# Kernel tuning notes

Hardware: AMD Instinct MI355X
Metric: run time of the kernel (lower is better)

## Reference

```python
import jax, jax.numpy as jnp
import numpy as np

SEQ, N, D, E = 16, 50000, 128, 1600000  # seq_len, n_nodes (lstm batch), feature dim, n_edges


def setup_inputs() -> dict:
    key = jax.random.key(0)
    ks = jax.random.split(key, 12)
    s = 1.0 / np.sqrt(D)

    def unif(k, shape):
        return jax.random.uniform(k, shape, jnp.float32, -s, s)

    return {
        "input_aux": jax.random.normal(ks[0], (SEQ, N, D), jnp.float32),
        "edges": jax.random.randint(ks[1], (2, E), 0, N, dtype=jnp.int64),
        # PyTorch LSTM params (single layer): gates ordered [i, f, g, o]
        "W_ih": unif(ks[2], (4 * D, D)),
        "W_hh": unif(ks[3], (4 * D, D)),
        "b_ih": unif(ks[4], (4 * D,)),
        "b_hh": unif(ks[5], (4 * D,)),
        # GCNConv layers (normalize=False): x' = scatter_sum((x @ W)[src] -> dst) + b
        "W1": unif(ks[6], (D, D)),
        "b1": unif(ks[7], (D,)),
        "W2": unif(ks[8], (D, D)),
        "b2": unif(ks[9], (D,)),
    }


def _lstm_last_hidden(x, W_ih, W_hh, b_ih, b_hh):
    # x: [T, N, D] (batch_first=False). Returns final hidden state h_T: [N, H].
    H = W_hh.shape[1]
    b = b_ih + b_hh

    def step(carry, xt):
        h, c = carry
        gates = xt @ W_ih.T + h @ W_hh.T + b  # [N, 4H]
        i, f, g, o = jnp.split(gates, 4, axis=-1)
        i = jax.nn.sigmoid(i)
        f = jax.nn.sigmoid(f)
        g = jnp.tanh(g)
        o = jax.nn.sigmoid(o)
        c = f * c + i * g
        h = o * jnp.tanh(c)
        return (h, c), None

    h0 = jnp.zeros((x.shape[1], H), x.dtype)
    (h, _), _ = jax.lax.scan(step, (h0, h0), x)
    return h


def _gcn_conv(x, edges, W, b):
    # GCNConv with normalize=False: transform, gather from source, scatter-sum to target, add bias.
    xw = x @ W                                    # [N, D]
    msg = xw[edges[0]]                            # [E, D] gather
    out = jax.ops.segment_sum(msg, edges[1], num_segments=x.shape[0])  # [N, D] scatter
    return out + b


def reference(input_aux, W_ih, W_hh, b_ih, b_hh, W1, b1, W2, b2, edges):
    h = _lstm_last_hidden(input_aux, W_ih, W_hh, b_ih, b_hh)  # squeeze(hn): [N, D]
    x = jax.nn.relu(_gcn_conv(h, edges, W1, b1))
    return _gcn_conv(x, edges, W2, b2)
```

## Files before the change

### kernel.cpp

```cpp
#include <hip/hip_runtime.h>
#include <hip/hip_bf16.h>

#define D 128
#define G4 512
#define KK 256

typedef __attribute__((ext_vector_type(4))) float f32x4;
typedef __attribute__((ext_vector_type(8))) __bf16 bf16x8;
typedef __attribute__((ext_vector_type(8))) unsigned short u16x8;
typedef __attribute__((ext_vector_type(4))) unsigned int u32x4;

__device__ __forceinline__ float sigm2(float x) {
    return __builtin_amdgcn_rcpf(1.0f + __builtin_amdgcn_exp2f(-1.4426950408889634f * x));
}
__device__ __forceinline__ float tanh2(float x) {
    return 1.0f - 2.0f * __builtin_amdgcn_rcpf(1.0f + __builtin_amdgcn_exp2f(2.8853900817779268f * x));
}
__device__ __forceinline__ float bf_lo(unsigned int u) { return __uint_as_float(u << 16); }
__device__ __forceinline__ float bf_hi(unsigned int u) { return __uint_as_float(u & 0xffff0000u); }

__global__ void k_prep(const float* __restrict__ Wih, const float* __restrict__ Whh,
                       const float* __restrict__ bih, const float* __restrict__ bhh,
                       const float* __restrict__ W1, const float* __restrict__ W2,
                       __bf16* __restrict__ Wcomb, __bf16* __restrict__ W1t,
                       __bf16* __restrict__ W2t, float* __restrict__ bcomb) {
    int t = blockIdx.x * blockDim.x + threadIdx.x;
    if (t < G4 * KK) {
        int row = t / KK, k = t % KK;
        float v = (k < D) ? Wih[row * D + k] : Whh[row * D + (k - D)];
        Wcomb[t] = (__bf16)v;
    } else if (t < G4 * KK + D * D) {
        int u = t - G4 * KK; int o = u / D, k = u % D;
        W1t[u] = (__bf16)W1[k * D + o];
    } else if (t < G4 * KK + 2 * D * D) {
        int u = t - G4 * KK - D * D; int o = u / D, k = u % D;
        W2t[u] = (__bf16)W2[k * D + o];
    } else if (t < G4 * KK + 2 * D * D + G4) {
        int u = t - G4 * KK - 2 * D * D;
        bcomb[u] = bih[u] + bhh[u];
    }
}

__global__ __launch_bounds__(512, 1) void k_lstm3(
        const float* __restrict__ xin, const __bf16* __restrict__ Wcomb,
        const float* __restrict__ bcomb, const __bf16* __restrict__ W1t,
        __bf16* __restrict__ xw1, int n, int tsteps, int npairs, int nchunks) {
    __shared__ __bf16 xb[2][2][16][D];
    __shared__ __bf16 hb[2][2][16][D];

    const int tid = threadIdx.x;
    const int wid = tid >> 6, l = tid & 63, q = l >> 4, c16 = l & 15;
    const int dim = wid * 16 + c16;

    bf16x8 Wf[4][8];
#pragma unroll
    for (int g = 0; g < 4; ++g)
#pragma unroll
        for (int kb = 0; kb < 8; ++kb)
            Wf[g][kb] = *(const bf16x8*)(Wcomb + (size_t)(g * D + dim) * KK + kb * 32 + q * 8);
#pragma unroll
    for (int g = 0; g < 4; ++g)
#pragma unroll
        for (int kb = 0; kb < 8; ++kb) {
            f32x4 tmp = __builtin_bit_cast(f32x4, Wf[g][kb]);
            asm volatile("" : "+v"(tmp));
            Wf[g][kb] = __builtin_bit_cast(bf16x8, tmp);
        }

    const float bI = bcomb[0 * D + dim], bF = bcomb[1 * D + dim],
                bG = bcomb[2 * D + dim], bO = bcomb[3 * D + dim];

    const int sid = tid >> 8;
    const int su = tid & 255;
    const int srow = su >> 4, sc8 = (su & 15) * 8;
    const int fin = tsteps & 1;

    for (int p = blockIdx.x; p < npairs; p += gridDim.x) {
        const int cA = 2 * p, cB = 2 * p + 1;
        const bool hasB = (cB < nchunks);
        const int myc = sid ? (hasB ? cB : cA) : cA;

        ((float4*)&hb[sid][0][0][0])[su] = make_float4(0.f, 0.f, 0.f, 0.f);
        {
            const float* xp = xin + ((size_t)(myc * 16 + srow)) * D + sc8;
            float4 v0 = *(const float4*)xp, v1 = *(const float4*)(xp + 4);
            bf16x8 b;
            b[0] = (__bf16)v0.x; b[1] = (__bf16)v0.y; b[2] = (__bf16)v0.z; b[3] = (__bf16)v0.w;
            b[4] = (__bf16)v1.x; b[5] = (__bf16)v1.y; b[6] = (__bf16)v1.z; b[7] = (__bf16)v1.w;
            *(bf16x8*)&xb[sid][0][srow][sc8 ^ ((srow & 7) << 3)] = b;
        }
        __syncthreads();

        float csA[4] = {0.f, 0.f, 0.f, 0.f}, csB[4] = {0.f, 0.f, 0.f, 0.f};

        for (int t = 0; t < tsteps; ++t) {
            const int cur = t & 1, nxt = cur ^ 1;

            bf16x8 aA[8], aB[8];
#pragma unroll
            for (int kb = 0; kb < 4; ++kb) {
                const int e = (kb * 32 + q * 8) ^ ((c16 & 7) << 3);
                aA[kb]     = *(const bf16x8*)&xb[0][cur][c16][e];
                aA[4 + kb] = *(const bf16x8*)&hb[0][cur][c16][e];
                aB[kb]     = *(const bf16x8*)&xb[1][cur][c16][e];
                aB[4 + kb] = *(const bf16x8*)&hb[1][cur][c16][e];
            }

            float4 p0, p1;
            const bool pf = (t + 1 < tsteps);
            if (pf) {
                const float* xp = xin + ((size_t)(t + 1) * n + myc * 16 + srow) * D + sc8;
                p0 = *(const float4*)xp; p1 = *(const float4*)(xp + 4);
            }

            f32x4 accA[4] = {{0,0,0,0},{0,0,0,0},{0,0,0,0},{0,0,0,0}};
            f32x4 accB[4] = {{0,0,0,0},{0,0,0,0},{0,0,0,0},{0,0,0,0}};
#pragma unroll
            for (int kb = 0; kb < 8; ++kb)
#pragma unroll
                for (int g = 0; g < 4; ++g) {
                    accA[g] = __builtin_amdgcn_mfma_f32_16x16x32_bf16(aA[kb], Wf[g][kb], accA[g], 0, 0, 0);
                    accB[g] = __builtin_amdgcn_mfma_f32_16x16x32_bf16(aB[kb], Wf[g][kb], accB[g], 0, 0, 0);
                }

            if (pf) {
                bf16x8 b;
                b[0] = (__bf16)p0.x; b[1] = (__bf16)p0.y; b[2] = (__bf16)p0.z; b[3] = (__bf16)p0.w;
                b[4] = (__bf16)p1.x; b[5] = (__bf16)p1.y; b[6] = (__bf16)p1.z; b[7] = (__bf16)p1.w;
                *(bf16x8*)&xb[sid][nxt][srow][sc8 ^ ((srow & 7) << 3)] = b;
            }

#pragma unroll
            for (int j = 0; j < 4; ++j) {
                const int node = j + q * 4;
                {
                    float iv = sigm2(accA[0][j] + bI);
                    float fv = sigm2(accA[1][j] + bF);
                    float gv = tanh2(accA[2][j] + bG);
                    float ov = sigm2(accA[3][j] + bO);
                    float c = fv * csA[j] + iv * gv;
                    csA[j] = c;
                    hb[0][nxt][node][dim ^ ((node & 7) << 3)] = (__bf16)(ov * tanh2(c));
                }
                {
                    float iv = sigm2(accB[0][j] + bI);
                    float fv = sigm2(accB[1][j] + bF);
                    float gv = tanh2(accB[2][j] + bG);
                    float ov = sigm2(accB[3][j] + bO);
                    float c = fv * csB[j] + iv * gv;
                    csB[j] = c;
                    hb[1][nxt][node][dim ^ ((node & 7) << 3)] = (__bf16)(ov * tanh2(c));
                }
            }
            __syncthreads();
        }

        bf16x8 hA[4], hB[4];
#pragma unroll
        for (int kb = 0; kb < 4; ++kb) {
            const int e = (kb * 32 + q * 8) ^ ((c16 & 7) << 3);
            hA[kb] = *(const bf16x8*)&hb[0][fin][c16][e];
            hB[kb] = *(const bf16x8*)&hb[1][fin][c16][e];
        }
        f32x4 eA = {0,0,0,0}, eB = {0,0,0,0};
#pragma unroll
        for (int kb = 0; kb < 4; ++kb) {
            bf16x8 wf = *(const bf16x8*)(W1t + (size_t)dim * D + kb * 32 + q * 8);
            eA = __builtin_amdgcn_mfma_f32_16x16x32_bf16(hA[kb], wf, eA, 0, 0, 0);
            eB = __builtin_amdgcn_mfma_f32_16x16x32_bf16(hB[kb], wf, eB, 0, 0, 0);
        }
#pragma unroll
        for (int j = 0; j < 4; ++j) {
            const int node = j + q * 4;
            xb[0][1][node][dim] = (__bf16)eA[j];
            xb[1][1][node][dim] = (__bf16)eB[j];
        }
        __syncthreads();
        if (!(sid == 1 && !hasB))
            *(bf16x8*)(xw1 + (size_t)(myc * 16 + srow) * D + sc8) = *(const bf16x8*)&xb[sid][1][srow][sc8];
        __syncthreads();
    }
}

__global__ __launch_bounds__(256) void k_gemm2(
        const __bf16* __restrict__ in, const __bf16* __restrict__ Wt,
        __bf16* __restrict__ outm, int n) {
    const int tid = threadIdx.x, wid = tid >> 6, l = tid & 63, q = l >> 4, c16 = l & 15;
    const int R = (blockIdx.x * 4 + wid) * 16;
    if (R + 16 > n) return;
    bf16x8 af[4];
#pragma unroll
    for (int kb = 0; kb < 4; ++kb)
        af[kb] = *(const bf16x8*)(in + (size_t)(R + c16) * D + kb * 32 + q * 8);
#pragma unroll
    for (int nt = 0; nt < 8; ++nt) {
        f32x4 acc = {0, 0, 0, 0};
#pragma unroll
        for (int kb = 0; kb < 4; ++kb) {
            const __bf16* wb = Wt + (size_t)(nt * 16 + c16) * D + (kb * 32 + q * 8);
            acc = __builtin_amdgcn_mfma_f32_16x16x32_bf16(af[kb], *(const bf16x8*)wb, acc, 0, 0, 0);
        }
#pragma unroll
        for (int j = 0; j < 4; ++j)
            outm[(size_t)(R + q * 4 + j) * D + nt * 16 + c16] = (__bf16)acc[j];
    }
}

__global__ void k_hist(const int* __restrict__ dst, int* __restrict__ counts, int e) {
    for (int i = blockIdx.x * blockDim.x + threadIdx.x; i < e; i += gridDim.x * blockDim.x)
        atomicAdd(&counts[dst[i]], 1);
}
__global__ __launch_bounds__(1024) void k_scan1(const int* __restrict__ counts,
        int* __restrict__ offsets, int* __restrict__ bsum, int n) {
    __shared__ int sd[1024];
    int tid = threadIdx.x, i = blockIdx.x * 1024 + tid;
    int v = (i < n) ? counts[i] : 0;
    sd[tid] = v; __syncthreads();
    for (int off = 1; off < 1024; off <<= 1) {
        int t = (tid >= off) ? sd[tid - off] : 0; __syncthreads();
        sd[tid] += t; __syncthreads();
    }
    if (i < n) offsets[i] = sd[tid] - v;
    if (tid == 1023) bsum[blockIdx.x] = sd[1023];
}
__global__ void k_scan2(const int* __restrict__ bsum, int* __restrict__ bpref, int nb) {
    if (threadIdx.x == 0) {
        int run = 0;
        for (int i = 0; i < nb; ++i) { bpref[i] = run; run += bsum[i]; }
    }
}
__global__ __launch_bounds__(1024) void k_scan3(int* __restrict__ offsets,
        int* __restrict__ cursor, const int* __restrict__ bpref, int n, int e) {
    int i = blockIdx.x * 1024 + threadIdx.x;
    if (i < n) {
        int v = offsets[i] + bpref[blockIdx.x];
        offsets[i] = v; cursor[i] = v;
    }
    if (i == 0) offsets[n] = e;
}
__global__ void k_permute(const int* __restrict__ src, const int* __restrict__ dst,
                          int* cursor, int* __restrict__ csr, int e) {
    for (int i = blockIdx.x * blockDim.x + threadIdx.x; i < e; i += gridDim.x * blockDim.x) {
        int p = atomicAdd(&cursor[dst[i]], 1);
        csr[p] = src[i];
    }
}

template <bool OUT_F32, bool RELU>
__global__ __launch_bounds__(256) void k_gather3(const __bf16* __restrict__ xw,
        const int* __restrict__ offsets, const int* __restrict__ csr,
        const float* __restrict__ bias, void* __restrict__ outp, int n) {
    const int gg = (blockIdx.x << 4) | (threadIdx.x >> 4);
    const int l = threadIdx.x & 15;
    if (gg >= n) return;
    const int s = offsets[gg], e = offsets[gg + 1];
    const u32x4* __restrict__ xq = (const u32x4*)xw;
    float a[8] = {0,0,0,0,0,0,0,0};
    int i = s;
    for (; i + 4 <= e; i += 4) {
        u32x4 v0 = xq[(size_t)csr[i]     * 16 + l];
        u32x4 v1 = xq[(size_t)csr[i + 1] * 16 + l];
        u32x4 v2 = xq[(size_t)csr[i + 2] * 16 + l];
        u32x4 v3 = xq[(size_t)csr[i + 3] * 16 + l];
#pragma unroll
        for (int k = 0; k < 4; ++k) {
            a[2 * k]     += (bf_lo(v0[k]) + bf_lo(v1[k])) + (bf_lo(v2[k]) + bf_lo(v3[k]));
            a[2 * k + 1] += (bf_hi(v0[k]) + bf_hi(v1[k])) + (bf_hi(v2[k]) + bf_hi(v3[k]));
        }
    }
    for (; i < e; ++i) {
        u32x4 v = xq[(size_t)csr[i] * 16 + l];
#pragma unroll
        for (int k = 0; k < 4; ++k) { a[2 * k] += bf_lo(v[k]); a[2 * k + 1] += bf_hi(v[k]); }
    }
    const float4 b0 = *(const float4*)(bias + l * 8);
    const float4 b1 = *(const float4*)(bias + l * 8 + 4);
    float r[8] = {a[0] + b0.x, a[1] + b0.y, a[2] + b0.z, a[3] + b0.w,
                  a[4] + b1.x, a[5] + b1.y, a[6] + b1.z, a[7] + b1.w};
    if (RELU) {
#pragma unroll
        for (int k = 0; k < 8; ++k) r[k] = fmaxf(r[k], 0.f);
    }
    if (OUT_F32) {
        float* o = (float*)outp + (size_t)gg * D + l * 8;
        *(float4*)o       = make_float4(r[0], r[1], r[2], r[3]);
        *(float4*)(o + 4) = make_float4(r[4], r[5], r[6], r[7]);
    } else {
        bf16x8 b;
#pragma unroll
        for (int k = 0; k < 8; ++k) b[k] = (__bf16)r[k];
        *(bf16x8*)((__bf16*)outp + (size_t)gg * D + l * 8) = b;
    }
}

extern "C" void kernel_launch(void* const* d_in, const int* in_sizes, int n_in,
                              void* d_out, int out_size, void* d_ws, size_t ws_size,
                              hipStream_t stream) {
    const float* xin = (const float*)d_in[0];
    const int*   edges = (const int*)d_in[1];
    const float* Wih = (const float*)d_in[2];
    const float* Whh = (const float*)d_in[3];
    const float* bih = (const float*)d_in[4];
    const float* bhh = (const float*)d_in[5];
    const float* W1  = (const float*)d_in[6];
    const float* b1  = (const float*)d_in[7];
    const float* W2  = (const float*)d_in[8];
    const float* b2  = (const float*)d_in[9];
    float* outp = (float*)d_out;

    const int E = in_sizes[1] / 2;
    const int n = out_size / D;
    const int tsteps = in_sizes[0] / (n * D);
    const int* srcE = edges;
    const int* dstE = edges + E;

    char* ws = (char*)d_ws;
    size_t off = 0;
    auto alloc = [&](size_t bytes) { void* p = ws + off; off += (bytes + 511) & ~(size_t)511; return p; };
    __bf16* Wcomb = (__bf16*)alloc((size_t)G4 * KK * 2);
    __bf16* W1t   = (__bf16*)alloc((size_t)D * D * 2);
    __bf16* W2t   = (__bf16*)alloc((size_t)D * D * 2);
    float*  bcomb = (float*)alloc((size_t)G4 * 4);
    int* counts  = (int*)alloc((size_t)(n + 1) * 4);
    int* offsets = (int*)alloc((size_t)(n + 1) * 4);
    int* cursor  = (int*)alloc((size_t)(n + 1) * 4);
    int* bsum    = (int*)alloc(64 * 4);
    int* bpref   = (int*)alloc(64 * 4);
    int* csr     = (int*)alloc((size_t)E * 4);
    __bf16* xw1  = (__bf16*)alloc((size_t)n * D * 2);
    __bf16* out1 = (__bf16*)alloc((size_t)n * D * 2);
    __bf16* xw2  = xw1;
    (void)ws_size; (void)n_in;

    {
        int total = G4 * KK + 2 * D * D + G4;
        k_prep<<<(total + 255) / 256, 256, 0, stream>>>(Wih, Whh, bih, bhh, W1, W2,
                                                        Wcomb, W1t, W2t, bcomb);
    }
    hipMemsetAsync(counts, 0, (size_t)n * 4, stream);
    k_hist<<<2048, 256, 0, stream>>>(dstE, counts, E);
    int nb = (n + 1023) / 1024;
    k_scan1<<<nb, 1024, 0, stream>>>(counts, offsets, bsum, n);
    k_scan2<<<1, 64, 0, stream>>>(bsum, bpref, nb);
    k_scan3<<<nb, 1024, 0, stream>>>(offsets, cursor, bpref, n, E);
    k_permute<<<2048, 256, 0, stream>>>(srcE, dstE, cursor, csr, E);

    const int nchunks = n / 16;
    const int npairs = (nchunks + 1) / 2;
    k_lstm3<<<256, 512, 0, stream>>>(xin, Wcomb, bcomb, W1t, xw1, n, tsteps, npairs, nchunks);

    k_gather3<false, true><<<(n + 15) / 16, 256, 0, stream>>>(xw1, offsets, csr, b1, out1, n);
    k_gemm2<<<((n / 16) + 3) / 4, 256, 0, stream>>>(out1, W2t, xw2, n);
    k_gather3<true, false><<<(n + 15) / 16, 256, 0, stream>>>(xw2, offsets, csr, b2, outp, n);
}
```

Measured before the change: 1.043 ms.

## Restructure LSTM kernel with AGPR weights, transposed MFMA, padded LDS, wider gather unroll

The LSTM kernel now pins the recurrent weights in accumulator registers through inline-asm MFMA, and swaps operand order so each lane writes four consecutive hidden dims as one vector store. It also replaces the XOR swizzle with padded LDS rows, seeds the accumulators with biases held in shared memory, unrolls the time loop by two, and raises launch bounds to allow two blocks per CU. The GCN gather now issues eight neighbor loads per iteration to raise memory-level parallelism. Risks include register pressure from the doubled occupancy target, the hand-placed s_nop hazard padding, and the time loop assuming an even tsteps.

```diff
diff --git a/kernel.cpp b/kernel.cpp
--- a/kernel.cpp
+++ b/kernel.cpp
@@ -4,11 +4,17 @@
 #define D 128
 #define G4 512
 #define KK 256
+#define LROW 144
 
 typedef __attribute__((ext_vector_type(4))) float f32x4;
 typedef __attribute__((ext_vector_type(8))) __bf16 bf16x8;
-typedef __attribute__((ext_vector_type(8))) unsigned short u16x8;
+typedef __attribute__((ext_vector_type(4))) __bf16 bf16x4;
 typedef __attribute__((ext_vector_type(4))) unsigned int u32x4;
+
+#define MFMA_AV(acc, wf, xf) \
+    asm volatile("v_mfma_f32_16x16x32_bf16 %0, %1, %2, %0" : "+v"(acc) : "a"(wf), "v"(xf))
+#define MFMA_VV(acc, wf, xf) \
+    asm volatile("v_mfma_f32_16x16x32_bf16 %0, %1, %2, %0" : "+v"(acc) : "v"(wf), "v"(xf))
 
 __device__ __forceinline__ float sigm2(float x) {
     return __builtin_amdgcn_rcpf(1.0f + __builtin_amdgcn_exp2f(-1.4426950408889634f * x));
@@ -41,143 +47,144 @@
     }
 }
 
-__global__ __launch_bounds__(512, 1) void k_lstm3(
+__global__ __launch_bounds__(512, 2) void k_lstm4(
         const float* __restrict__ xin, const __bf16* __restrict__ Wcomb,
         const float* __restrict__ bcomb, const __bf16* __restrict__ W1t,
         __bf16* __restrict__ xw1, int n, int tsteps, int npairs, int nchunks) {
-    __shared__ __bf16 xb[2][2][16][D];
-    __shared__ __bf16 hb[2][2][16][D];
+    __shared__ __align__(16) float  sbias[G4];
+    __shared__ __align__(16) __bf16 xb[2][2][16][LROW];
+    __shared__ __align__(16) __bf16 hb[2][2][16][LROW];
 
     const int tid = threadIdx.x;
     const int wid = tid >> 6, l = tid & 63, q = l >> 4, c16 = l & 15;
-    const int dim = wid * 16 + c16;
+    const int q8 = q * 8;
+    const int wrow = wid * 16 + c16;
+    const int w16q4 = wid * 16 + q * 4;
 
     bf16x8 Wf[4][8];
 #pragma unroll
     for (int g = 0; g < 4; ++g)
 #pragma unroll
         for (int kb = 0; kb < 8; ++kb)
-            Wf[g][kb] = *(const bf16x8*)(Wcomb + (size_t)(g * D + dim) * KK + kb * 32 + q * 8);
-#pragma unroll
-    for (int g = 0; g < 4; ++g)
-#pragma unroll
-        for (int kb = 0; kb < 8; ++kb) {
-            f32x4 tmp = __builtin_bit_cast(f32x4, Wf[g][kb]);
-            asm volatile("" : "+v"(tmp));
-            Wf[g][kb] = __builtin_bit_cast(bf16x8, tmp);
-        }
-
-    const float bI = bcomb[0 * D + dim], bF = bcomb[1 * D + dim],
-                bG = bcomb[2 * D + dim], bO = bcomb[3 * D + dim];
+            Wf[g][kb] = *(const bf16x8*)(Wcomb + (size_t)(g * D + wrow) * KK + kb * 32 + q8);
+
+    if (tid < G4) sbias[tid] = bcomb[tid];
 
     const int sid = tid >> 8;
     const int su = tid & 255;
     const int srow = su >> 4, sc8 = (su & 15) * 8;
-    const int fin = tsteps & 1;
 
     for (int p = blockIdx.x; p < npairs; p += gridDim.x) {
         const int cA = 2 * p, cB = 2 * p + 1;
         const bool hasB = (cB < nchunks);
         const int myc = sid ? (hasB ? cB : cA) : cA;
 
-        ((float4*)&hb[sid][0][0][0])[su] = make_float4(0.f, 0.f, 0.f, 0.f);
         {
+            bf16x8 z = {};
+            *(bf16x8*)&hb[sid][0][srow][sc8] = z;
             const float* xp = xin + ((size_t)(myc * 16 + srow)) * D + sc8;
             float4 v0 = *(const float4*)xp, v1 = *(const float4*)(xp + 4);
             bf16x8 b;
             b[0] = (__bf16)v0.x; b[1] = (__bf16)v0.y; b[2] = (__bf16)v0.z; b[3] = (__bf16)v0.w;
             b[4] = (__bf16)v1.x; b[5] = (__bf16)v1.y; b[6] = (__bf16)v1.z; b[7] = (__bf16)v1.w;
-            *(bf16x8*)&xb[sid][0][srow][sc8 ^ ((srow & 7) << 3)] = b;
+            *(bf16x8*)&xb[sid][0][srow][sc8] = b;
         }
         __syncthreads();
 
         float csA[4] = {0.f, 0.f, 0.f, 0.f}, csB[4] = {0.f, 0.f, 0.f, 0.f};
 
-        for (int t = 0; t < tsteps; ++t) {
-            const int cur = t & 1, nxt = cur ^ 1;
-
-            bf16x8 aA[8], aB[8];
-#pragma unroll
-            for (int kb = 0; kb < 4; ++kb) {
-                const int e = (kb * 32 + q * 8) ^ ((c16 & 7) << 3);
-                aA[kb]     = *(const bf16x8*)&xb[0][cur][c16][e];
-                aA[4 + kb] = *(const bf16x8*)&hb[0][cur][c16][e];
-                aB[kb]     = *(const bf16x8*)&xb[1][cur][c16][e];
-                aB[4 + kb] = *(const bf16x8*)&hb[1][cur][c16][e];
+        for (int t0 = 0; t0 < tsteps; t0 += 2) {
+#pragma unroll
+            for (int tt = 0; tt < 2; ++tt) {
+                const int t = t0 + tt, cur = tt, nxt = tt ^ 1;
+
+                f32x4 accA[4], accB[4];
+#pragma unroll
+                for (int g = 0; g < 4; ++g) {
+                    accA[g] = *(const f32x4*)&sbias[g * D + w16q4];
+                    accB[g] = accA[g];
+                }
+
+                float4 px0, px1;
+                const bool pf = (t + 1 < tsteps);
+                if (pf) {
+                    const float* xp = xin + ((size_t)(t + 1) * n + myc * 16 + srow) * D + sc8;
+                    px0 = *(const float4*)xp; px1 = *(const float4*)(xp + 4);
+                }
+
+#pragma unroll
+                for (int kb = 0; kb < 8; ++kb) {
+                    const int e = (kb & 3) * 32 + q8;
+                    bf16x8 fA, fB;
+                    if (kb < 4) {
+                        fA = *(const bf16x8*)&xb[0][cur][c16][e];
+                        fB = *(const bf16x8*)&xb[1][cur][c16][e];
+                    } else {
+                        fA = *(const bf16x8*)&hb[0][cur][c16][e];
+                        fB = *(const bf16x8*)&hb[1][cur][c16][e];
+                    }
+                    MFMA_AV(accA[0], Wf[0][kb], fA); MFMA_AV(accB[0], Wf[0][kb], fB);
+                    MFMA_AV(accA[1], Wf[1][kb], fA); MFMA_AV(accB[1], Wf[1][kb], fB);
+                    MFMA_AV(accA[2], Wf[2][kb], fA); MFMA_AV(accB[2], Wf[2][kb], fB);
+                    MFMA_AV(accA[3], Wf[3][kb], fA); MFMA_AV(accB[3], Wf[3][kb], fB);
+                }
+                asm volatile("s_nop 7\n\ts_nop 7");
+
+                if (pf) {
+                    bf16x8 b;
+                    b[0] = (__bf16)px0.x; b[1] = (__bf16)px0.y; b[2] = (__bf16)px0.z; b[3] = (__bf16)px0.w;
+                    b[4] = (__bf16)px1.x; b[5] = (__bf16)px1.y; b[6] = (__bf16)px1.z; b[7] = (__bf16)px1.w;
+                    *(bf16x8*)&xb[sid][nxt][srow][sc8] = b;
+                }
+
+                {
+                    bf16x4 hv;
+#pragma unroll
+                    for (int j = 0; j < 4; ++j) {
+                        float iv = sigm2(accA[0][j]);
+                        float fv = sigm2(accA[1][j]);
+                        float gv = tanh2(accA[2][j]);
+                        float ov = sigm2(accA[3][j]);
+                        float c = fv * csA[j] + iv * gv;
+                        csA[j] = c;
+                        hv[j] = (__bf16)(ov * tanh2(c));
+                    }
+                    *(bf16x4*)&hb[0][nxt][c16][w16q4] = hv;
+                }
+                {
+                    bf16x4 hv;
+#pragma unroll
+                    for (int j = 0; j < 4; ++j) {
+                        float iv = sigm2(accB[0][j]);
+                        float fv = sigm2(accB[1][j]);
+                        float gv = tanh2(accB[2][j]);
+                        float ov = sigm2(accB[3][j]);
+                        float c = fv * csB[j] + iv * gv;
+                        csB[j] = c;
+                        hv[j] = (__bf16)(ov * tanh2(c));
+                    }
+                    *(bf16x4*)&hb[1][nxt][c16][w16q4] = hv;
+                }
+                __syncthreads();
             }
-
-            float4 p0, p1;
-            const bool pf = (t + 1 < tsteps);
-            if (pf) {
-                const float* xp = xin + ((size_t)(t + 1) * n + myc * 16 + srow) * D + sc8;
-                p0 = *(const float4*)xp; p1 = *(const float4*)(xp + 4);
-            }
-
-            f32x4 accA[4] = {{0,0,0,0},{0,0,0,0},{0,0,0,0},{0,0,0,0}};
-            f32x4 accB[4] = {{0,0,0,0},{0,0,0,0},{0,0,0,0},{0,0,0,0}};
-#pragma unroll
-            for (int kb = 0; kb < 8; ++kb)
-#pragma unroll
-                for (int g = 0; g < 4; ++g) {
-                    accA[g] = __builtin_amdgcn_mfma_f32_16x16x32_bf16(aA[kb], Wf[g][kb], accA[g], 0, 0, 0);
-                    accB[g] = __builtin_amdgcn_mfma_f32_16x16x32_bf16(aB[kb], Wf[g][kb], accB[g], 0, 0, 0);
-                }
-
-            if (pf) {
-                bf16x8 b;
-                b[0] = (__bf16)p0.x; b[1] = (__bf16)p0.y; b[2] = (__bf16)p0.z; b[3] = (__bf16)p0.w;
-                b[4] = (__bf16)p1.x; b[5] = (__bf16)p1.y; b[6] = (__bf16)p1.z; b[7] = (__bf16)p1.w;
-                *(bf16x8*)&xb[sid][nxt][srow][sc8 ^ ((srow & 7) << 3)] = b;
-            }
-
-#pragma unroll
-            for (int j = 0; j < 4; ++j) {
-                const int node = j + q * 4;
-                {
-                    float iv = sigm2(accA[0][j] + bI);
-                    float fv = sigm2(accA[1][j] + bF);
-                    float gv = tanh2(accA[2][j] + bG);
-                    float ov = sigm2(accA[3][j] + bO);
-                    float c = fv * csA[j] + iv * gv;
-                    csA[j] = c;
-                    hb[0][nxt][node][dim ^ ((node & 7) << 3)] = (__bf16)(ov * tanh2(c));
-                }
-                {
-                    float iv = sigm2(accB[0][j] + bI);
-                    float fv = sigm2(accB[1][j] + bF);
-                    float gv = tanh2(accB[2][j] + bG);
-                    float ov = sigm2(accB[3][j] + bO);
-                    float c = fv * csB[j] + iv * gv;
-                    csB[j] = c;
-                    hb[1][nxt][node][dim ^ ((node & 7) << 3)] = (__bf16)(ov * tanh2(c));
-                }
-            }
-            __syncthreads();
-        }
-
-        bf16x8 hA[4], hB[4];
+        }
+
+        f32x4 eA = {0, 0, 0, 0}, eB = {0, 0, 0, 0};
 #pragma unroll
         for (int kb = 0; kb < 4; ++kb) {
-            const int e = (kb * 32 + q * 8) ^ ((c16 & 7) << 3);
-            hA[kb] = *(const bf16x8*)&hb[0][fin][c16][e];
-            hB[kb] = *(const bf16x8*)&hb[1][fin][c16][e];
-        }
-        f32x4 eA = {0,0,0,0}, eB = {0,0,0,0};
-#pragma unroll
-        for (int kb = 0; kb < 4; ++kb) {
-            bf16x8 wf = *(const bf16x8*)(W1t + (size_t)dim * D + kb * 32 + q * 8);
-            eA = __builtin_amdgcn_mfma_f32_16x16x32_bf16(hA[kb], wf, eA, 0, 0, 0);
-            eB = __builtin_amdgcn_mfma_f32_16x16x32_bf16(hB[kb], wf, eB, 0, 0, 0);
-        }
-#pragma unroll
-        for (int j = 0; j < 4; ++j) {
-            const int node = j + q * 4;
-            xb[0][1][node][dim] = (__bf16)eA[j];
-            xb[1][1][node][dim] = (__bf16)eB[j];
-        }
-        __syncthreads();
-        if (!(sid == 1 && !hasB))
-            *(bf16x8*)(xw1 + (size_t)(myc * 16 + srow) * D + sc8) = *(const bf16x8*)&xb[sid][1][srow][sc8];
+            bf16x8 w1f = *(const bf16x8*)(W1t + (size_t)wrow * D + kb * 32 + q8);
+            bf16x8 hA = *(const bf16x8*)&hb[0][0][c16][kb * 32 + q8];
+            bf16x8 hB = *(const bf16x8*)&hb[1][0][c16][kb * 32 + q8];
+            MFMA_VV(eA, w1f, hA);
+            MFMA_VV(eB, w1f, hB);
+        }
+        asm volatile("s_nop 7\n\ts_nop 7");
+        bf16x4 oA, oB;
+#pragma unroll
+        for (int j = 0; j < 4; ++j) { oA[j] = (__bf16)eA[j]; oB[j] = (__bf16)eB[j]; }
+        *(bf16x4*)(xw1 + (size_t)(cA * 16 + c16) * D + w16q4) = oA;
+        if (hasB)
+            *(bf16x4*)(xw1 + (size_t)(cB * 16 + c16) * D + w16q4) = oB;
         __syncthreads();
     }
 }
@@ -257,18 +264,28 @@
     const u32x4* __restrict__ xq = (const u32x4*)xw;
     float a[8] = {0,0,0,0,0,0,0,0};
     int i = s;
-    for (; i + 4 <= e; i += 4) {
-        u32x4 v0 = xq[(size_t)csr[i]     * 16 + l];
+    for (; i + 8 <= e; i += 8) {
+        u32x4 v[8];
+#pragma unroll
+        for (int r = 0; r < 8; ++r) v[r] = xq[(size_t)csr[i + r] * 16 + l];
+#pragma unroll
+        for (int r = 0; r < 8; ++r)
+#pragma unroll
+            for (int k = 0; k < 4; ++k) {
+                a[2 * k]     += bf_lo(v[r][k]);
+                a[2 * k + 1] += bf_hi(v[r][k]);
+            }
+    }
+    for (; i + 2 <= e; i += 2) {
+        u32x4 v0 = xq[(size_t)csr[i] * 16 + l];
         u32x4 v1 = xq[(size_t)csr[i + 1] * 16 + l];
-        u32x4 v2 = xq[(size_t)csr[i + 2] * 16 + l];
-        u32x4 v3 = xq[(size_t)csr[i + 3] * 16 + l];
 #pragma unroll
         for (int k = 0; k < 4; ++k) {
-            a[2 * k]     += (bf_lo(v0[k]) + bf_lo(v1[k])) + (bf_lo(v2[k]) + bf_lo(v3[k]));
-            a[2 * k + 1] += (bf_hi(v0[k]) + bf_hi(v1[k])) + (bf_hi(v2[k]) + bf_hi(v3[k]));
-        }
-    }
-    for (; i < e; ++i) {
+            a[2 * k]     += bf_lo(v0[k]) + bf_lo(v1[k]);
+            a[2 * k + 1] += bf_hi(v0[k]) + bf_hi(v1[k]);
+        }
+    }
+    if (i < e) {
         u32x4 v = xq[(size_t)csr[i] * 16 + l];
 #pragma unroll
         for (int k = 0; k < 4; ++k) { a[2 * k] += bf_lo(v[k]); a[2 * k + 1] += bf_hi(v[k]); }
@@ -347,7 +364,7 @@
 
     const int nchunks = n / 16;
     const int npairs = (nchunks + 1) / 2;
-    k_lstm3<<<256, 512, 0, stream>>>(xin, Wcomb, bcomb, W1t, xw1, n, tsteps, npairs, nchunks);
+    k_lstm4<<<256, 512, 0, stream>>>(xin, Wcomb, bcomb, W1t, xw1, n, tsteps, npairs, nchunks);
 
     k_gather3<false, true><<<(n + 15) / 16, 256, 0, stream>>>(xw1, offsets, csr, b1, out1, n);
     k_gemm2<<<((n / 16) + 3) / 4, 256, 0, stream>>>(out1, W2t, xw2, n);
```

Result: no change. 1.026 ms (-1.7%).
